# Performance work log

Measured on AMD Instinct MI355X. Metric: run time of the kernel, lower is better.

## Reference

```python
import jax, jax.numpy as jnp
import numpy as np

NUM_HEADS = 16

def setup_inputs() -> dict:
    key = jax.random.key(0)
    ks = jax.random.split(key, 5)
    b, n, d = 2, 2048, 1024
    s = 0.02
    return {
        "x": jax.random.normal(ks[0], (b, n, d), jnp.float32),
        "wq": jax.random.normal(ks[1], (d, d), jnp.float32) * s,
        "wk": jax.random.normal(ks[2], (d, d), jnp.float32) * s,
        "wv": jax.random.normal(ks[3], (d, d), jnp.float32) * s,
        "wo": jax.random.normal(ks[4], (d, d), jnp.float32) * s,
        "bo": jnp.zeros((d,), jnp.float32),
    }

def reference(x, wq, wk, wv, wo, bo):
    b, n, c = x.shape
    h = NUM_HEADS
    hd = c // h
    scale = hd ** -0.5
    # qkv projections (qkv_bias=False); torch Linear computes x @ W.T
    def split_heads(t):
        return t.reshape(b, n, h, hd).transpose(0, 2, 1, 3)  # b h n d
    q = split_heads(x @ wq.T)
    k = split_heads(x @ wk.T)
    v = split_heads(x @ wv.T)
    dots = jnp.einsum('bhid,bhjd->bhij', q, k) * scale
    attn = jax.nn.softmax(dots, axis=-1)  # attn_drop=0 -> identity
    out = jnp.einsum('bhij,bhjd->bhid', attn, v)
    out = out.transpose(0, 2, 1, 3).reshape(b, n, c)
    out = out @ wo.T + bo  # proj_drop=0 -> identity
    return out
```

## Files before the change

### kernel.cpp

```cpp
#include <hip/hip_runtime.h>
#include <hip/hip_bf16.h>

typedef float f32x4 __attribute__((ext_vector_type(4)));
typedef short short8 __attribute__((ext_vector_type(8)));
typedef short short4v __attribute__((ext_vector_type(4)));

#define MFMA(a, b, c) __builtin_amdgcn_mfma_f32_16x16x32_bf16((a), (b), (c), 0, 0, 0)

#if __has_builtin(__builtin_amdgcn_exp2f)
#define EXP2(x) __builtin_amdgcn_exp2f(x)
#else
#define EXP2(x) exp2f(x)
#endif

#define B_  2
#define N_  2048
#define C_  1024
#define H_  16
#define HD_ 64
#define M_  (B_ * N_)

#define QSCALE 0.18033688011112042f

typedef const __attribute__((address_space(1))) void* gp_t;
typedef __attribute__((address_space(3))) void* sp_t;
#define GLL16(g, s) __builtin_amdgcn_global_load_lds((gp_t)(const void*)(g), (sp_t)(void*)(s), 16, 0, 0)

__device__ __forceinline__ short f2bf(float f) {
    union { float fv; unsigned u; } v; v.fv = f;
    unsigned r = v.u + 0x7fffu + ((v.u >> 16) & 1u);
    return (short)(r >> 16);
}
__device__ __forceinline__ unsigned pack_rne(float a, float b) {
    return (unsigned)(unsigned short)f2bf(a) | ((unsigned)(unsigned short)f2bf(b) << 16);
}

__global__ __launch_bounds__(256) void convert_kernel(
    const float* __restrict__ x,  const float* __restrict__ wq,
    const float* __restrict__ wk, const float* __restrict__ wv,
    const float* __restrict__ wo, short* __restrict__ dst)
{
    size_t e = ((size_t)blockIdx.x * 256 + threadIdx.x) * 8;
    const float* src; size_t off;
    if (e < 4194304)      { src = x;  off = e; }
    else if (e < 5242880) { src = wq; off = e - 4194304; }
    else if (e < 6291456) { src = wk; off = e - 5242880; }
    else if (e < 7340032) { src = wv; off = e - 6291456; }
    else                  { src = wo; off = e - 7340032; }
    float4 a = *(const float4*)(src + off);
    float4 b = *(const float4*)(src + off + 4);
    short8 s;
    s[0] = f2bf(a.x); s[1] = f2bf(a.y); s[2] = f2bf(a.z); s[3] = f2bf(a.w);
    s[4] = f2bf(b.x); s[5] = f2bf(b.y); s[6] = f2bf(b.z); s[7] = f2bf(b.w);
    *(short8*)(dst + e) = s;
}

__global__ __launch_bounds__(256) void qkv_gemm(
    const short* __restrict__ xb, const short* __restrict__ Wb,
    short* __restrict__ Qb, short* __restrict__ Kb, short* __restrict__ Vt)
{
    const int m0 = blockIdx.x * 128;
    const int n0 = blockIdx.y * 128;
    __shared__ short As[128 * 64];
    __shared__ short Bs[128 * 64];
    const int tid  = threadIdx.x;
    const int wave = tid >> 6, lane = tid & 63;
    const int quad = lane >> 4, l16 = lane & 15;
    const int wr = (wave >> 1) * 64, wc = (wave & 1) * 64;
    const int sw = l16 & 7;

    const int rS = tid >> 3;
    const int cS = (tid & 7) ^ (rS & 7);
    const short* A_src = xb + (size_t)(m0 + rS) * C_ + cS * 8;
    const short* B_src = Wb + (size_t)(n0 + rS) * C_ + cS * 8;

    f32x4 acc[4][4] = {};

    for (int kk = 0; kk < C_; kk += 64) {
        __syncthreads();
        #pragma unroll
        for (int it = 0; it < 4; ++it) {
            GLL16(A_src + (size_t)(it * 32) * C_ + kk, &As[it * 2048 + tid * 8]);
            GLL16(B_src + (size_t)(it * 32) * C_ + kk, &Bs[it * 2048 + tid * 8]);
        }
        __syncthreads();
        short8 af[4][2], bf[4][2];
        #pragma unroll
        for (int mi = 0; mi < 4; ++mi) {
            int row = (wr + mi * 16 + l16) * 64;
            af[mi][0] = *(const short8*)&As[row + ((quad    ) ^ sw) * 8];
            af[mi][1] = *(const short8*)&As[row + ((quad + 4) ^ sw) * 8];
        }
        #pragma unroll
        for (int ni = 0; ni < 4; ++ni) {
            int row = (wc + ni * 16 + l16) * 64;
            bf[ni][0] = *(const short8*)&Bs[row + ((quad    ) ^ sw) * 8];
            bf[ni][1] = *(const short8*)&Bs[row + ((quad + 4) ^ sw) * 8];
        }
        #pragma unroll
        for (int k2 = 0; k2 < 2; ++k2)
        #pragma unroll
        for (int mi = 0; mi < 4; ++mi)
        #pragma unroll
        for (int ni = 0; ni < 4; ++ni)
            acc[mi][ni] = MFMA(af[mi][k2], bf[ni][k2], acc[mi][ni]);
    }

    const int which = n0 >> 10;
    const int nb = n0 & 1023;
    #pragma unroll
    for (int mi = 0; mi < 4; ++mi)
    #pragma unroll
    for (int ni = 0; ni < 4; ++ni)
    #pragma unroll
    for (int r = 0; r < 4; ++r) {
        int m  = m0 + wr + mi * 16 + quad * 4 + r;
        int cc = nb + wc + ni * 16 + l16;
        float av = acc[mi][ni][r];
        if (which == 0) av *= QSCALE;
        short bv = f2bf(av);
        int bb = m >> 11, ns = m & (N_ - 1);
        int h = cc >> 6, d = cc & 63;
        size_t bh = (size_t)(bb * H_ + h);
        if (which == 0)      Qb[(bh * N_ + ns) * HD_ + d] = bv;
        else if (which == 1) Kb[(bh * N_ + ns) * HD_ + d] = bv;
        else                 Vt[(bh * HD_ + d) * N_ + ns] = bv;
    }
}

__global__ __launch_bounds__(256, 5) void attn_kernel(
    const short* __restrict__ Qb, const short* __restrict__ Kb,
    const short* __restrict__ Vt, short* __restrict__ Ob)
{
    const int bid = blockIdx.y * 32 + blockIdx.x;
    const int swz = (bid & 7) * 128 + (bid >> 3);
    const int bh = swz >> 5;
    const int i0 = (swz & 31) * 64;
    const int b = bh >> 4, h = bh & (H_ - 1);
    __shared__ short Ks[2][64 * 64];
    __shared__ short Vs[2][64 * 64];
    const int tid  = threadIdx.x;
    const int wave = tid >> 6, lane = tid & 63;
    const int quad = lane >> 4, l16 = lane & 15;
    const int sw = l16 & 7;

    const short* Qg = Qb + ((size_t)bh * N_ + i0) * HD_;
    const short* Kg = Kb + (size_t)bh * N_ * HD_;
    const short* Vg = Vt + (size_t)bh * HD_ * N_;

    const int row0 = tid >> 3,  c0 = (tid & 7) ^ (row0 & 7);
    const int row1 = row0 + 32, c1 = (tid & 7) ^ (row1 & 7);
    const short* KgA0 = Kg + row0 * HD_ + c0 * 8;
    const short* KgA1 = Kg + row1 * HD_ + c1 * 8;
    const short* VgA0 = Vg + (size_t)row0 * N_ + c0 * 8;
    const short* VgA1 = Vg + (size_t)row1 * N_ + c1 * 8;

    short8 qf[2];
    {
        const short* qrow = Qg + (wave * 16 + l16) * HD_;
        qf[0] = *(const short8*)(qrow + quad * 8);
        qf[1] = *(const short8*)(qrow + quad * 8 + 32);
    }

    GLL16(KgA0, &Ks[0][tid * 8]);
    GLL16(KgA1, &Ks[0][(tid + 256) * 8]);
    GLL16(VgA0, &Vs[0][tid * 8]);
    GLL16(VgA1, &Vs[0][(tid + 256) * 8]);
    __syncthreads();

    f32x4 o[4] = {};
    float lrow = 0.f;

    for (int jt = 0; jt < N_ / 64; ++jt) {
        const int cur = jt & 1;
        if (jt + 1 < N_ / 64) {
            int j1 = (jt + 1) * 64;
            GLL16(KgA0 + (size_t)j1 * HD_, &Ks[cur ^ 1][tid * 8]);
            GLL16(KgA1 + (size_t)j1 * HD_, &Ks[cur ^ 1][(tid + 256) * 8]);
            GLL16(VgA0 + j1, &Vs[cur ^ 1][tid * 8]);
            GLL16(VgA1 + j1, &Vs[cur ^ 1][(tid + 256) * 8]);
        }
        const short* Kc = Ks[cur];
        const short* Vc = Vs[cur];

        #pragma unroll
        for (int half = 0; half < 2; ++half) {
            unsigned pq[4];
            #pragma unroll
            for (int nio = 0; nio < 2; ++nio) {
                int ni = half * 2 + nio;
                int krow = (ni * 16 + l16) * 64;
                short8 kf0 = *(const short8*)&Kc[krow + ((quad ^ sw) * 8)];
                short8 kf1 = *(const short8*)&Kc[krow + (((quad + 4) ^ sw) * 8)];
                f32x4 st = {0.f, 0.f, 0.f, 0.f};
                __builtin_amdgcn_s_setprio(1);
                st = MFMA(kf0, qf[0], st);
                st = MFMA(kf1, qf[1], st);
                __builtin_amdgcn_s_setprio(0);
                union { float f; unsigned u; } e0, e1, e2, e3;
                e0.f = EXP2(st[0]); e1.f = EXP2(st[1]);
                e2.f = EXP2(st[2]); e3.f = EXP2(st[3]);
                lrow += (e0.f + e1.f) + (e2.f + e3.f);
                pq[nio * 2]     = __builtin_amdgcn_perm(e1.u, e0.u, 0x07060302u);
                pq[nio * 2 + 1] = __builtin_amdgcn_perm(e3.u, e2.u, 0x07060302u);
            }
            #pragma unroll
            for (int di = 0; di < 4; ++di) {
                int vrow = (di * 16 + l16) * 64;
                int ch1 = (half * 4 +     (quad >> 1)) ^ sw;
                int ch2 = (half * 4 + 2 + (quad >> 1)) ^ sw;
                union { struct { short4v lo, hi; } p; short8 v; } va;
                va.p.lo = *(const short4v*)&Vc[vrow + ch1 * 8 + (quad & 1) * 4];
                va.p.hi = *(const short4v*)&Vc[vrow + ch2 * 8 + (quad & 1) * 4];
                union { unsigned u[4]; short8 v; } pb;
                pb.u[0] = pq[0]; pb.u[1] = pq[1];
                pb.u[2] = pq[2]; pb.u[3] = pq[3];
                __builtin_amdgcn_s_setprio(1);
                o[di] = MFMA(va.v, pb.v, o[di]);
                __builtin_amdgcn_s_setprio(0);
            }
        }
        __syncthreads();
    }

    {
        float l = lrow;
        l += __shfl_xor(l, 16, 64);
        l += __shfl_xor(l, 32, 64);
        float inv = 1.f / l;
        int ig = i0 + wave * 16 + l16;
        size_t base = ((size_t)(b * N_ + ig)) * C_ + h * HD_;
        #pragma unroll
        for (int di = 0; di < 4; ++di) {
            unsigned p01 = pack_rne(o[di][0] * inv, o[di][1] * inv);
            unsigned p23 = pack_rne(o[di][2] * inv, o[di][3] * inv);
            *(unsigned*)&Ob[base + di * 16 + quad * 4]     = p01;
            *(unsigned*)&Ob[base + di * 16 + quad * 4 + 2] = p23;
        }
    }
}

__global__ __launch_bounds__(256) void proj_gemm(
    const short* __restrict__ Ob, const short* __restrict__ wob,
    const float* __restrict__ bo, float* __restrict__ out)
{
    const int m0 = blockIdx.x * 64;
    const int n0 = blockIdx.y * 128;
    __shared__ short As[64 * 64];
    __shared__ short Bs[128 * 64];
    const int tid  = threadIdx.x;
    const int wave = tid >> 6, lane = tid & 63;
    const int quad = lane >> 4, l16 = lane & 15;
    const int wr = (wave >> 1) * 32, wc = (wave & 1) * 64;
    const int sw = l16 & 7;

    const int rS = tid >> 3;
    const int cS = (tid & 7) ^ (rS & 7);
    const short* A_src = Ob  + (size_t)(m0 + rS) * C_ + cS * 8;
    const short* B_src = wob + (size_t)(n0 + rS) * C_ + cS * 8;

    f32x4 acc[2][4] = {};

    for (int kk = 0; kk < C_; kk += 64) {
        __syncthreads();
        GLL16(A_src + kk, &As[tid * 8]);
        GLL16(A_src + (size_t)32 * C_ + kk, &As[(tid + 256) * 8]);
        #pragma unroll
        for (int it = 0; it < 4; ++it)
            GLL16(B_src + (size_t)(it * 32) * C_ + kk, &Bs[it * 2048 + tid * 8]);
        __syncthreads();
        short8 af[2][2], bf[4][2];
        #pragma unroll
        for (int mi = 0; mi < 2; ++mi) {
            int row = (wr + mi * 16 + l16) * 64;
            af[mi][0] = *(const short8*)&As[row + ((quad    ) ^ sw) * 8];
            af[mi][1] = *(const short8*)&As[row + ((quad + 4) ^ sw) * 8];
        }
        #pragma unroll
        for (int ni = 0; ni < 4; ++ni) {
            int row = (wc + ni * 16 + l16) * 64;
            bf[ni][0] = *(const short8*)&Bs[row + ((quad    ) ^ sw) * 8];
            bf[ni][1] = *(const short8*)&Bs[row + ((quad + 4) ^ sw) * 8];
        }
        #pragma unroll
        for (int k2 = 0; k2 < 2; ++k2)
        #pragma unroll
        for (int mi = 0; mi < 2; ++mi)
        #pragma unroll
        for (int ni = 0; ni < 4; ++ni)
            acc[mi][ni] = MFMA(af[mi][k2], bf[ni][k2], acc[mi][ni]);
    }

    #pragma unroll
    for (int mi = 0; mi < 2; ++mi)
    #pragma unroll
    for (int ni = 0; ni < 4; ++ni)
    #pragma unroll
    for (int r = 0; r < 4; ++r) {
        int m = m0 + wr + mi * 16 + quad * 4 + r;
        int c = n0 + wc + ni * 16 + l16;
        out[(size_t)m * C_ + c] = acc[mi][ni][r] + bo[c];
    }
}

extern "C" void kernel_launch(void* const* d_in, const int* in_sizes, int n_in,
                              void* d_out, int out_size, void* d_ws, size_t ws_size,
                              hipStream_t stream) {
    const float* x  = (const float*)d_in[0];
    const float* wq = (const float*)d_in[1];
    const float* wk = (const float*)d_in[2];
    const float* wv = (const float*)d_in[3];
    const float* wo = (const float*)d_in[4];
    const float* bo = (const float*)d_in[5];
    float* out = (float*)d_out;

    short* xb  = (short*)d_ws;
    short* Wb  = xb  + 4194304;
    short* wob = Wb  + 3145728;
    short* Qb  = wob + 1048576;
    short* Kb  = Qb  + 4194304;
    short* Vt  = Kb  + 4194304;
    short* Obuf= Vt  + 4194304;

    dim3 blk(256);
    convert_kernel<<<4096, blk, 0, stream>>>(x, wq, wk, wv, wo, xb);
    qkv_gemm<<<dim3(M_ / 128, 3072 / 128), blk, 0, stream>>>(xb, Wb, Qb, Kb, Vt);
    attn_kernel<<<dim3(N_ / 64, B_ * H_), blk, 0, stream>>>(Qb, Kb, Vt, Obuf);
    proj_gemm<<<dim3(M_ / 64, C_ / 128), blk, 0, stream>>>(Obuf, wob, bo, out);
}
```

Before: 191.6 us.

## Split attention over key halves with fp32 partials and a merge kernel

```diff
diff --git a/kernel.cpp b/kernel.cpp
--- a/kernel.cpp
+++ b/kernel.cpp
@@ -128,15 +128,16 @@
     }
 }
 
-__global__ __launch_bounds__(256, 5) void attn_kernel(
+__global__ __launch_bounds__(256, 5) void attn_split(
     const short* __restrict__ Qb, const short* __restrict__ Kb,
-    const short* __restrict__ Vt, short* __restrict__ Ob)
-{
-    const int bid = blockIdx.y * 32 + blockIdx.x;
-    const int swz = (bid & 7) * 128 + (bid >> 3);
-    const int bh = swz >> 5;
-    const int i0 = (swz & 31) * 64;
-    const int b = bh >> 4, h = bh & (H_ - 1);
+    const short* __restrict__ Vt, float* __restrict__ Opart,
+    float* __restrict__ lpart)
+{
+    const int bid = blockIdx.x;
+    const int swz = (bid & 7) * 256 + (bid >> 3);
+    const int bh = swz >> 6;
+    const int i0 = ((swz >> 1) & 31) * 64;
+    const int sp = swz & 1;
     __shared__ short Ks[2][64 * 64];
     __shared__ short Vs[2][64 * 64];
     const int tid  = threadIdx.x;
@@ -150,10 +151,10 @@
 
     const int row0 = tid >> 3,  c0 = (tid & 7) ^ (row0 & 7);
     const int row1 = row0 + 32, c1 = (tid & 7) ^ (row1 & 7);
-    const short* KgA0 = Kg + row0 * HD_ + c0 * 8;
-    const short* KgA1 = Kg + row1 * HD_ + c1 * 8;
-    const short* VgA0 = Vg + (size_t)row0 * N_ + c0 * 8;
-    const short* VgA1 = Vg + (size_t)row1 * N_ + c1 * 8;
+    const short* KgA0 = Kg + (sp * 1024 + row0) * HD_ + c0 * 8;
+    const short* KgA1 = Kg + (sp * 1024 + row1) * HD_ + c1 * 8;
+    const short* VgA0 = Vg + (size_t)row0 * N_ + sp * 1024 + c0 * 8;
+    const short* VgA1 = Vg + (size_t)row1 * N_ + sp * 1024 + c1 * 8;
 
     short8 qf[2];
     {
@@ -171,9 +172,9 @@
     f32x4 o[4] = {};
     float lrow = 0.f;
 
-    for (int jt = 0; jt < N_ / 64; ++jt) {
+    for (int jt = 0; jt < 16; ++jt) {
         const int cur = jt & 1;
-        if (jt + 1 < N_ / 64) {
+        if (jt + 1 < 16) {
             int j1 = (jt + 1) * 64;
             GLL16(KgA0 + (size_t)j1 * HD_, &Ks[cur ^ 1][tid * 8]);
             GLL16(KgA1 + (size_t)j1 * HD_, &Ks[cur ^ 1][(tid + 256) * 8]);
@@ -227,6 +228,136 @@
         float l = lrow;
         l += __shfl_xor(l, 16, 64);
         l += __shfl_xor(l, 32, 64);
+        int ig = i0 + wave * 16 + l16;
+        float* obase = Opart + ((size_t)(sp * 32 + bh) * N_ + ig) * HD_;
+        #pragma unroll
+        for (int di = 0; di < 4; ++di)
+            *(f32x4*)(obase + di * 16 + quad * 4) = o[di];
+        if (quad == 0) lpart[sp * 65536 + bh * N_ + ig] = l;
+    }
+}
+
+__global__ __launch_bounds__(256) void merge_kernel(
+    const float* __restrict__ Opart, const float* __restrict__ lpart,
+    short* __restrict__ Ob)
+{
+    int e8 = (blockIdx.x * 256 + threadIdx.x) * 8;
+    int bh = e8 >> 17;
+    int rem = e8 & 131071;
+    int ig = rem >> 6, d = rem & 63;
+    f32x4 a0 = *(const f32x4*)(Opart + e8);
+    f32x4 a1 = *(const f32x4*)(Opart + e8 + 4);
+    f32x4 b0 = *(const f32x4*)(Opart + 4194304 + e8);
+    f32x4 b1 = *(const f32x4*)(Opart + 4194304 + e8 + 4);
+    float inv = 1.f / (lpart[bh * N_ + ig] + lpart[65536 + bh * N_ + ig]);
+    short8 s;
+    s[0] = f2bf((a0[0] + b0[0]) * inv); s[1] = f2bf((a0[1] + b0[1]) * inv);
+    s[2] = f2bf((a0[2] + b0[2]) * inv); s[3] = f2bf((a0[3] + b0[3]) * inv);
+    s[4] = f2bf((a1[0] + b1[0]) * inv); s[5] = f2bf((a1[1] + b1[1]) * inv);
+    s[6] = f2bf((a1[2] + b1[2]) * inv); s[7] = f2bf((a1[3] + b1[3]) * inv);
+    int b = bh >> 4, h = bh & (H_ - 1);
+    *(short8*)&Ob[((size_t)(b * N_ + ig)) * C_ + h * HD_ + d] = s;
+}
+
+__global__ __launch_bounds__(256, 5) void attn_full(
+    const short* __restrict__ Qb, const short* __restrict__ Kb,
+    const short* __restrict__ Vt, short* __restrict__ Ob)
+{
+    const int bid = blockIdx.y * 32 + blockIdx.x;
+    const int swz = (bid & 7) * 128 + (bid >> 3);
+    const int bh = swz >> 5;
+    const int i0 = (swz & 31) * 64;
+    const int b = bh >> 4, h = bh & (H_ - 1);
+    __shared__ short Ks[2][64 * 64];
+    __shared__ short Vs[2][64 * 64];
+    const int tid  = threadIdx.x;
+    const int wave = tid >> 6, lane = tid & 63;
+    const int quad = lane >> 4, l16 = lane & 15;
+    const int sw = l16 & 7;
+
+    const short* Qg = Qb + ((size_t)bh * N_ + i0) * HD_;
+    const short* Kg = Kb + (size_t)bh * N_ * HD_;
+    const short* Vg = Vt + (size_t)bh * HD_ * N_;
+
+    const int row0 = tid >> 3,  c0 = (tid & 7) ^ (row0 & 7);
+    const int row1 = row0 + 32, c1 = (tid & 7) ^ (row1 & 7);
+    const short* KgA0 = Kg + row0 * HD_ + c0 * 8;
+    const short* KgA1 = Kg + row1 * HD_ + c1 * 8;
+    const short* VgA0 = Vg + (size_t)row0 * N_ + c0 * 8;
+    const short* VgA1 = Vg + (size_t)row1 * N_ + c1 * 8;
+
+    short8 qf[2];
+    {
+        const short* qrow = Qg + (wave * 16 + l16) * HD_;
+        qf[0] = *(const short8*)(qrow + quad * 8);
+        qf[1] = *(const short8*)(qrow + quad * 8 + 32);
+    }
+
+    GLL16(KgA0, &Ks[0][tid * 8]);
+    GLL16(KgA1, &Ks[0][(tid + 256) * 8]);
+    GLL16(VgA0, &Vs[0][tid * 8]);
+    GLL16(VgA1, &Vs[0][(tid + 256) * 8]);
+    __syncthreads();
+
+    f32x4 o[4] = {};
+    float lrow = 0.f;
+
+    for (int jt = 0; jt < N_ / 64; ++jt) {
+        const int cur = jt & 1;
+        if (jt + 1 < N_ / 64) {
+            int j1 = (jt + 1) * 64;
+            GLL16(KgA0 + (size_t)j1 * HD_, &Ks[cur ^ 1][tid * 8]);
+            GLL16(KgA1 + (size_t)j1 * HD_, &Ks[cur ^ 1][(tid + 256) * 8]);
+            GLL16(VgA0 + j1, &Vs[cur ^ 1][tid * 8]);
+            GLL16(VgA1 + j1, &Vs[cur ^ 1][(tid + 256) * 8]);
+        }
+        const short* Kc = Ks[cur];
+        const short* Vc = Vs[cur];
+
+        #pragma unroll
+        for (int half = 0; half < 2; ++half) {
+            unsigned pq[4];
+            #pragma unroll
+            for (int nio = 0; nio < 2; ++nio) {
+                int ni = half * 2 + nio;
+                int krow = (ni * 16 + l16) * 64;
+                short8 kf0 = *(const short8*)&Kc[krow + ((quad ^ sw) * 8)];
+                short8 kf1 = *(const short8*)&Kc[krow + (((quad + 4) ^ sw) * 8)];
+                f32x4 st = {0.f, 0.f, 0.f, 0.f};
+                __builtin_amdgcn_s_setprio(1);
+                st = MFMA(kf0, qf[0], st);
+                st = MFMA(kf1, qf[1], st);
+                __builtin_amdgcn_s_setprio(0);
+                union { float f; unsigned u; } e0, e1, e2, e3;
+                e0.f = EXP2(st[0]); e1.f = EXP2(st[1]);
+                e2.f = EXP2(st[2]); e3.f = EXP2(st[3]);
+                lrow += (e0.f + e1.f) + (e2.f + e3.f);
+                pq[nio * 2]     = __builtin_amdgcn_perm(e1.u, e0.u, 0x07060302u);
+                pq[nio * 2 + 1] = __builtin_amdgcn_perm(e3.u, e2.u, 0x07060302u);
+            }
+            #pragma unroll
+            for (int di = 0; di < 4; ++di) {
+                int vrow = (di * 16 + l16) * 64;
+                int ch1 = (half * 4 +     (quad >> 1)) ^ sw;
+                int ch2 = (half * 4 + 2 + (quad >> 1)) ^ sw;
+                union { struct { short4v lo, hi; } p; short8 v; } va;
+                va.p.lo = *(const short4v*)&Vc[vrow + ch1 * 8 + (quad & 1) * 4];
+                va.p.hi = *(const short4v*)&Vc[vrow + ch2 * 8 + (quad & 1) * 4];
+                union { unsigned u[4]; short8 v; } pb;
+                pb.u[0] = pq[0]; pb.u[1] = pq[1];
+                pb.u[2] = pq[2]; pb.u[3] = pq[3];
+                __builtin_amdgcn_s_setprio(1);
+                o[di] = MFMA(va.v, pb.v, o[di]);
+                __builtin_amdgcn_s_setprio(0);
+            }
+        }
+        __syncthreads();
+    }
+
+    {
+        float l = lrow;
+        l += __shfl_xor(l, 16, 64);
+        l += __shfl_xor(l, 32, 64);
         float inv = 1.f / l;
         int ig = i0 + wave * 16 + l16;
         size_t base = ((size_t)(b * N_ + ig)) * C_ + h * HD_;
@@ -321,10 +452,18 @@
     short* Kb  = Qb  + 4194304;
     short* Vt  = Kb  + 4194304;
     short* Obuf= Vt  + 4194304;
+    float* Opart = (float*)(Obuf + 4194304);
+    float* lpart = Opart + 2 * 4194304;
+    size_t need = (size_t)((char*)(lpart + 2 * 65536) - (char*)d_ws);
 
     dim3 blk(256);
     convert_kernel<<<4096, blk, 0, stream>>>(x, wq, wk, wv, wo, xb);
     qkv_gemm<<<dim3(M_ / 128, 3072 / 128), blk, 0, stream>>>(xb, Wb, Qb, Kb, Vt);
-    attn_kernel<<<dim3(N_ / 64, B_ * H_), blk, 0, stream>>>(Qb, Kb, Vt, Obuf);
+    if (ws_size >= need) {
+        attn_split<<<2048, blk, 0, stream>>>(Qb, Kb, Vt, Opart, lpart);
+        merge_kernel<<<2048, blk, 0, stream>>>(Opart, lpart, Obuf);
+    } else {
+        attn_full<<<dim3(N_ / 64, B_ * H_), blk, 0, stream>>>(Qb, Kb, Vt, Obuf);
+    }
     proj_gemm<<<dim3(M_ / 64, C_ / 128), blk, 0, stream>>>(Obuf, wob, bo, out);
 }
```

Result: slower. 196.1 us (+2.3%).

## Split attention over the key dimension into two partial halves and merge

Applied to the files above, without the earlier changes.

```diff
diff --git a/kernel.cpp b/kernel.cpp
--- a/kernel.cpp
+++ b/kernel.cpp
@@ -128,15 +128,16 @@
     }
 }
 
-__global__ __launch_bounds__(256, 5) void attn_kernel(
+__global__ __launch_bounds__(256, 5) void attn_split(
     const short* __restrict__ Qb, const short* __restrict__ Kb,
-    const short* __restrict__ Vt, short* __restrict__ Ob)
-{
-    const int bid = blockIdx.y * 32 + blockIdx.x;
-    const int swz = (bid & 7) * 128 + (bid >> 3);
-    const int bh = swz >> 5;
-    const int i0 = (swz & 31) * 64;
-    const int b = bh >> 4, h = bh & (H_ - 1);
+    const short* __restrict__ Vt, float* __restrict__ Opart,
+    float* __restrict__ lpart)
+{
+    const int bid = blockIdx.x;
+    const int swz = (bid & 7) * 256 + (bid >> 3);
+    const int bh = swz >> 6;
+    const int i0 = ((swz >> 1) & 31) * 64;
+    const int sp = swz & 1;
     __shared__ short Ks[2][64 * 64];
     __shared__ short Vs[2][64 * 64];
     const int tid  = threadIdx.x;
@@ -150,10 +151,10 @@
 
     const int row0 = tid >> 3,  c0 = (tid & 7) ^ (row0 & 7);
     const int row1 = row0 + 32, c1 = (tid & 7) ^ (row1 & 7);
-    const short* KgA0 = Kg + row0 * HD_ + c0 * 8;
-    const short* KgA1 = Kg + row1 * HD_ + c1 * 8;
-    const short* VgA0 = Vg + (size_t)row0 * N_ + c0 * 8;
-    const short* VgA1 = Vg + (size_t)row1 * N_ + c1 * 8;
+    const short* KgA0 = Kg + (sp * 1024 + row0) * HD_ + c0 * 8;
+    const short* KgA1 = Kg + (sp * 1024 + row1) * HD_ + c1 * 8;
+    const short* VgA0 = Vg + (size_t)row0 * N_ + sp * 1024 + c0 * 8;
+    const short* VgA1 = Vg + (size_t)row1 * N_ + sp * 1024 + c1 * 8;
 
     short8 qf[2];
     {
@@ -171,9 +172,9 @@
     f32x4 o[4] = {};
     float lrow = 0.f;
 
-    for (int jt = 0; jt < N_ / 64; ++jt) {
+    for (int jt = 0; jt < 16; ++jt) {
         const int cur = jt & 1;
-        if (jt + 1 < N_ / 64) {
+        if (jt + 1 < 16) {
             int j1 = (jt + 1) * 64;
             GLL16(KgA0 + (size_t)j1 * HD_, &Ks[cur ^ 1][tid * 8]);
             GLL16(KgA1 + (size_t)j1 * HD_, &Ks[cur ^ 1][(tid + 256) * 8]);
@@ -227,17 +228,35 @@
         float l = lrow;
         l += __shfl_xor(l, 16, 64);
         l += __shfl_xor(l, 32, 64);
-        float inv = 1.f / l;
         int ig = i0 + wave * 16 + l16;
-        size_t base = ((size_t)(b * N_ + ig)) * C_ + h * HD_;
-        #pragma unroll
-        for (int di = 0; di < 4; ++di) {
-            unsigned p01 = pack_rne(o[di][0] * inv, o[di][1] * inv);
-            unsigned p23 = pack_rne(o[di][2] * inv, o[di][3] * inv);
-            *(unsigned*)&Ob[base + di * 16 + quad * 4]     = p01;
-            *(unsigned*)&Ob[base + di * 16 + quad * 4 + 2] = p23;
-        }
-    }
+        float* obase = Opart + ((size_t)(sp * 32 + bh) * N_ + ig) * HD_;
+        #pragma unroll
+        for (int di = 0; di < 4; ++di)
+            *(f32x4*)(obase + di * 16 + quad * 4) = o[di];
+        if (quad == 0) lpart[sp * 65536 + bh * N_ + ig] = l;
+    }
+}
+
+__global__ __launch_bounds__(256) void merge_kernel(
+    const float* __restrict__ Opart, const float* __restrict__ lpart,
+    short* __restrict__ Ob)
+{
+    int e8 = (blockIdx.x * 256 + threadIdx.x) * 8;
+    int bh = e8 >> 17;
+    int rem = e8 & 131071;
+    int ig = rem >> 6, d = rem & 63;
+    f32x4 a0 = *(const f32x4*)(Opart + e8);
+    f32x4 a1 = *(const f32x4*)(Opart + e8 + 4);
+    f32x4 b0 = *(const f32x4*)(Opart + 4194304 + e8);
+    f32x4 b1 = *(const f32x4*)(Opart + 4194304 + e8 + 4);
+    float inv = 1.f / (lpart[bh * N_ + ig] + lpart[65536 + bh * N_ + ig]);
+    short8 s;
+    s[0] = f2bf((a0[0] + b0[0]) * inv); s[1] = f2bf((a0[1] + b0[1]) * inv);
+    s[2] = f2bf((a0[2] + b0[2]) * inv); s[3] = f2bf((a0[3] + b0[3]) * inv);
+    s[4] = f2bf((a1[0] + b1[0]) * inv); s[5] = f2bf((a1[1] + b1[1]) * inv);
+    s[6] = f2bf((a1[2] + b1[2]) * inv); s[7] = f2bf((a1[3] + b1[3]) * inv);
+    int b = bh >> 4, h = bh & (H_ - 1);
+    *(short8*)&Ob[((size_t)(b * N_ + ig)) * C_ + h * HD_ + d] = s;
 }
 
 __global__ __launch_bounds__(256) void proj_gemm(
@@ -321,10 +340,13 @@
     short* Kb  = Qb  + 4194304;
     short* Vt  = Kb  + 4194304;
     short* Obuf= Vt  + 4194304;
+    float* Opart = (float*)(Obuf + 4194304);
+    float* lpart = Opart + 2 * 4194304;
 
     dim3 blk(256);
     convert_kernel<<<4096, blk, 0, stream>>>(x, wq, wk, wv, wo, xb);
     qkv_gemm<<<dim3(M_ / 128, 3072 / 128), blk, 0, stream>>>(xb, Wb, Qb, Kb, Vt);
-    attn_kernel<<<dim3(N_ / 64, B_ * H_), blk, 0, stream>>>(Qb, Kb, Vt, Obuf);
+    attn_split<<<2048, blk, 0, stream>>>(Qb, Kb, Vt, Opart, lpart);
+    merge_kernel<<<2048, blk, 0, stream>>>(Opart, lpart, Obuf);
     proj_gemm<<<dim3(M_ / 64, C_ / 128), blk, 0, stream>>>(Obuf, wob, bo, out);
 }
```

Result: slower. 197.0 us (+2.8%).
